# Optimization experiments

Hardware: AMD Instinct MI355X
Metric: run time of the kernel (lower is better)

## Reference

```python
import jax, jax.numpy as jnp
import numpy as np

VOCAB = 29
VEC = 512      # vector_dim
HID = 1024     # hidden_size
SEN = 64       # sen_len (== seq length)
BATCH = 2048


def setup_inputs() -> dict:
    key = jax.random.key(0)
    k1, k2, k3, k4, k5, k6 = jax.random.split(key, 6)
    s_emb = 1.0
    s_ih = 1.0 / np.sqrt(HID)
    s_cls = 1.0 / np.sqrt(HID)
    return {
        "x": jax.random.randint(k1, (BATCH, SEN), 0, VOCAB, dtype=jnp.int64),
        "emb": jax.random.normal(k2, (VOCAB, VEC), dtype=jnp.float32) * s_emb,
        "W_ih": jax.random.uniform(k3, (HID, VEC), dtype=jnp.float32, minval=-s_ih, maxval=s_ih),
        "W_hh": jax.random.uniform(k4, (HID, HID), dtype=jnp.float32, minval=-s_ih, maxval=s_ih),
        "W_cls": jax.random.uniform(k5, (SEN + 1, HID), dtype=jnp.float32, minval=-s_cls, maxval=s_cls),
        "b_cls": jax.random.uniform(k6, (SEN + 1,), dtype=jnp.float32, minval=-s_cls, maxval=s_cls),
    }


def reference(x, emb, W_ih, W_hh, W_cls, b_cls):
    # Embedding lookup: [B, S, VEC]
    xe = emb[x]
    # Precompute input projections for all timesteps: [B, S, HID]
    xin = jnp.einsum("bsv,hv->bsh", xe, W_ih)

    def step(h, x_t):
        # h: [B, HID], x_t: [B, HID] (already W_ih @ x)
        h_new = jnp.tanh(x_t + h @ W_hh.T)
        return h_new, None

    h0 = jnp.zeros((x.shape[0], HID), dtype=xin.dtype)
    h_last, _ = jax.lax.scan(step, h0, jnp.swapaxes(xin, 0, 1))  # scan over S

    # h.squeeze() in torch (num_layers=1) -> [B, HID]
    logits = h_last @ W_cls.T + b_cls  # [B, SEN+1]
    return logits
```

## Files before the change

### kernel.cpp

```cpp
#include <hip/hip_runtime.h>
#include <hip/hip_bf16.h>

#define VOCAB 29
#define VEC   512
#define HID   1024
#define SEN   64
#define BATCH 2048

typedef __bf16 bf16_t;
typedef bf16_t bf16x8 __attribute__((ext_vector_type(8)));
typedef float  floatx4 __attribute__((ext_vector_type(4)));

__global__ void cvt_whh(const float* __restrict__ w, bf16_t* __restrict__ o, int n) {
    int i = blockIdx.x * blockDim.x + threadIdx.x;
    if (i < n) o[i] = (bf16_t)w[i];
}

__global__ void cvt_wcls(const float* __restrict__ w, bf16_t* __restrict__ o) {
    int i = blockIdx.x * blockDim.x + threadIdx.x;
    if (i >= 80 * HID) return;
    o[i] = (i < 65 * HID) ? (bf16_t)w[i] : (bf16_t)0.0f;
}

__global__ void proj_kernel(const float* __restrict__ emb, const float* __restrict__ wih,
                            float* __restrict__ proj) {
    int idx = blockIdx.x * blockDim.x + threadIdx.x;
    if (idx >= VOCAB * HID) return;
    int v = idx / HID, h = idx % HID;
    const float* e = emb + v * VEC;
    const float* w = wih + h * VEC;
    float s = 0.f;
    for (int k = 0; k < VEC; k += 4) {
        float4 ev = *(const float4*)(e + k);
        float4 wv = *(const float4*)(w + k);
        s += ev.x * wv.x + ev.y * wv.y + ev.z * wv.z + ev.w * wv.w;
    }
    proj[idx] = s;
}

__device__ __forceinline__ float fast_tanh(float x) {
    float e = __expf(2.0f * x);
    return 1.0f - 2.0f / (e + 1.0f);
}

__device__ __forceinline__ void load16_to_lds(const bf16_t* g, bf16_t* l) {
    auto gp = reinterpret_cast<const __attribute__((address_space(1))) unsigned int*>(
        reinterpret_cast<uintptr_t>(g));
    auto lp = reinterpret_cast<__attribute__((address_space(3))) unsigned int*>(
        static_cast<unsigned int>(reinterpret_cast<uintptr_t>(l)));
    __builtin_amdgcn_global_load_lds(gp, lp, 16, 0, 0);
}

#define BM 128
#define BN 64
#define PANEL_BLKS 16
#define SB() __builtin_amdgcn_sched_barrier(0)

#define ISSUE_AF(BUF, KBASE)                                                     \
    _Pragma("unroll")                                                            \
    for (int j = 0; j < 8; j++) {                                                \
        af[BUF][j][0] = *(const bf16x8*)(hA + ((KBASE) + j) * 32);               \
        af[BUF][j][1] = *(const bf16x8*)(hA + 16 * HID + ((KBASE) + j) * 32);    \
    }

#define COMPUTE_GROUP(BUF, KBASE)                                                \
    _Pragma("unroll")                                                            \
    for (int j = 0; j < 8; j++) {                                                \
        const int p = (4 * ((KBASE) + j) + q) ^ l7;   \
        bf16x8 b0 = *(const bf16x8*)&Bsh[l16][p * 8];                            \
        bf16x8 b1 = *(const bf16x8*)&Bsh[16 + l16][p * 8];                       \
        bf16x8 b2 = *(const bf16x8*)&Bsh[32 + l16][p * 8];                       \
        bf16x8 b3 = *(const bf16x8*)&Bsh[48 + l16][p * 8];                       \
        acc[0][0] = __builtin_amdgcn_mfma_f32_16x16x32_bf16(af[BUF][j][0], b0, acc[0][0], 0, 0, 0); \
        acc[0][1] = __builtin_amdgcn_mfma_f32_16x16x32_bf16(af[BUF][j][0], b1, acc[0][1], 0, 0, 0); \
        acc[0][2] = __builtin_amdgcn_mfma_f32_16x16x32_bf16(af[BUF][j][0], b2, acc[0][2], 0, 0, 0); \
        acc[0][3] = __builtin_amdgcn_mfma_f32_16x16x32_bf16(af[BUF][j][0], b3, acc[0][3], 0, 0, 0); \
        acc[1][0] = __builtin_amdgcn_mfma_f32_16x16x32_bf16(af[BUF][j][1], b0, acc[1][0], 0, 0, 0); \
        acc[1][1] = __builtin_amdgcn_mfma_f32_16x16x32_bf16(af[BUF][j][1], b1, acc[1][1], 0, 0, 0); \
        acc[1][2] = __builtin_amdgcn_mfma_f32_16x16x32_bf16(af[BUF][j][1], b2, acc[1][2], 0, 0, 0); \
        acc[1][3] = __builtin_amdgcn_mfma_f32_16x16x32_bf16(af[BUF][j][1], b3, acc[1][3], 0, 0, 0); \
    }

__global__ __launch_bounds__(256, 1)
void rnn_persist(const bf16_t* __restrict__ whh, const float* __restrict__ proj,
                 const int* __restrict__ x, bf16_t* hbuf, int* scnt)
{
    __shared__ __align__(16) bf16_t Bsh[BN][HID];
    __shared__ int uni_sh;

    const int tid  = threadIdx.x;
    const int m0   = blockIdx.x * BM;
    const int n0   = blockIdx.y * BN;
    const int wave = tid >> 6;
    const int lane = tid & 63;
    const int wm   = wave * 32;
    const int q    = lane >> 4;
    const int l16  = lane & 15;
    const int l7   = l16 & 7;

    int* cnt   = scnt + blockIdx.x * 64;
    int* xmask = scnt + (16 + blockIdx.x) * 64;
    int* fl    = scnt + 2048 + blockIdx.x * 64;

#pragma unroll
    for (int half = 0; half < 2; half++)
#pragma unroll
        for (int it = 0; it < 16; it++) {
            const int r = it * 4 + wave;
            load16_to_lds(whh + (n0 + r) * HID + half * 512 + (lane ^ (r & 7)) * 8,
                          &Bsh[r][half * 512 + lane * 8]);
        }

    int rowl[8];
#pragma unroll
    for (int mi = 0; mi < 2; mi++)
#pragma unroll
        for (int r = 0; r < 4; r++) rowl[mi * 4 + r] = m0 + wm + mi * 16 + q * 4 + r;

    {
        float pv0[8][4];
#pragma unroll
        for (int i = 0; i < 8; i++) {
            const int tok = x[rowl[i] * SEN + 0];
            const float* pr = proj + tok * HID + n0;
#pragma unroll
            for (int ni = 0; ni < 4; ni++) pv0[i][ni] = pr[ni * 16 + l16];
        }
#pragma unroll
        for (int i = 0; i < 8; i++)
#pragma unroll
            for (int ni = 0; ni < 4; ni++)
                hbuf[rowl[i] * HID + n0 + ni * 16 + l16] = (bf16_t)fast_tanh(pv0[i][ni]);
    }

    int tk[8];
#pragma unroll
    for (int i = 0; i < 8; i++) tk[i] = x[rowl[i] * SEN + 1];

    __syncthreads();
    if (tid == 0) {
        const int my_xcd = (int)__builtin_amdgcn_s_getreg((3 << 11) | 20);
        __hip_atomic_fetch_or(xmask, 1 << my_xcd, __ATOMIC_RELAXED, __HIP_MEMORY_SCOPE_AGENT);
        __hip_atomic_fetch_add(cnt, 1, __ATOMIC_RELEASE, __HIP_MEMORY_SCOPE_AGENT);
        while (__hip_atomic_load(cnt, __ATOMIC_ACQUIRE, __HIP_MEMORY_SCOPE_AGENT) < PANEL_BLKS)
            __builtin_amdgcn_s_sleep(1);
        const int m = __hip_atomic_load(xmask, __ATOMIC_RELAXED, __HIP_MEMORY_SCOPE_AGENT);
        uni_sh = ((m & (m - 1)) == 0);
    }
    __syncthreads();
    asm volatile("buffer_inv" ::: "memory");
    const int safe = !uni_sh;

#pragma unroll 1
    for (int t = 1; t < SEN; t++) {
        const bf16_t* h_in  = hbuf + (size_t)((t + 1) & 1) * (BATCH * HID);
        bf16_t*       h_out = hbuf + (size_t)(t & 1) * (BATCH * HID);

        floatx4 acc[2][4];
#pragma unroll
        for (int i = 0; i < 2; i++)
#pragma unroll
            for (int j = 0; j < 4; j++) acc[i][j] = (floatx4){0.f, 0.f, 0.f, 0.f};

        const bf16_t* hA = h_in + (m0 + wm + l16) * HID + q * 8;
        bf16x8 af[2][8][2];

        ISSUE_AF(0, 0)
        ISSUE_AF(1, 8)
        float pv[8][4];
#pragma unroll
        for (int i = 0; i < 8; i++) {
            const float* pr = proj + tk[i] * HID + n0;
#pragma unroll
            for (int ni = 0; ni < 4; ni++) pv[i][ni] = pr[ni * 16 + l16];
        }
        SB();
        COMPUTE_GROUP(0, 0)
        SB();
        ISSUE_AF(0, 16)
        SB();
        COMPUTE_GROUP(1, 8)
        SB();
        ISSUE_AF(1, 24)
        if (t < SEN - 1) {
#pragma unroll
            for (int i = 0; i < 8; i++) tk[i] = x[rowl[i] * SEN + t + 1];
        }
        SB();
        COMPUTE_GROUP(0, 16)
        SB();
        COMPUTE_GROUP(1, 24)
        SB();

#pragma unroll
        for (int mi = 0; mi < 2; mi++)
#pragma unroll
            for (int r = 0; r < 4; r++)
#pragma unroll
                for (int ni = 0; ni < 4; ni++) {
                    float v = acc[mi][ni][r] + pv[mi * 4 + r][ni];
                    h_out[rowl[mi * 4 + r] * HID + n0 + ni * 16 + l16] = (bf16_t)fast_tanh(v);
                }

        if (t < SEN - 1) {
            __syncthreads();
            if (safe) {
                if (tid == 0) {
                    __hip_atomic_fetch_add(cnt, 1, __ATOMIC_RELEASE, __HIP_MEMORY_SCOPE_AGENT);
                    while (__hip_atomic_load(cnt, __ATOMIC_ACQUIRE, __HIP_MEMORY_SCOPE_AGENT)
                           < PANEL_BLKS * (t + 1))
                        __builtin_amdgcn_s_sleep(1);
                }
            } else {
                if (tid == 0)
                    __hip_atomic_store(&fl[blockIdx.y], t,
                                       __ATOMIC_RELAXED, __HIP_MEMORY_SCOPE_AGENT);
                if (tid < 16) {
                    while (__hip_atomic_load(&fl[tid],
                                             __ATOMIC_RELAXED, __HIP_MEMORY_SCOPE_AGENT) < t) {}
                }
            }
            __syncthreads();
            asm volatile("buffer_inv" ::: "memory");
        }
    }
}

#undef ISSUE_AF
#undef COMPUTE_GROUP

#define CBM 128
#define CLDK 72
__global__ __launch_bounds__(256)
void classifier_mfma(const bf16_t* __restrict__ h, const bf16_t* __restrict__ wcls,
                     const float* __restrict__ bcls, float* __restrict__ out)
{
    __shared__ __align__(16) bf16_t Ash[CBM][CLDK];
    __shared__ __align__(16) bf16_t Bsh[80][CLDK];

    const int tid = threadIdx.x;
    const int m0 = blockIdx.x * CBM;
    const int wave = tid >> 6, lane = tid & 63;
    const int wm = wave * 32;
    const int q = lane >> 4, l16 = lane & 15;

    floatx4 acc[2][5];
#pragma unroll
    for (int i = 0; i < 2; i++)
#pragma unroll
        for (int j = 0; j < 5; j++) acc[i][j] = (floatx4){0.f, 0.f, 0.f, 0.f};

    for (int kk = 0; kk < HID; kk += 64) {
#pragma unroll
        for (int it = 0; it < 4; it++) {
            int idx = tid + it * 256, r = idx >> 3, c = (idx & 7) * 8;
            *(uint4*)&Ash[r][c] = *(const uint4*)&h[(m0 + r) * HID + kk + c];
        }
#pragma unroll
        for (int it = 0; it < 3; it++) {
            int idx = tid + it * 256;
            if (idx < 640) {
                int r = idx >> 3, c = (idx & 7) * 8;
                *(uint4*)&Bsh[r][c] = *(const uint4*)&wcls[r * HID + kk + c];
            }
        }
        __syncthreads();
#pragma unroll
        for (int ks = 0; ks < 64; ks += 32) {
            bf16x8 af[2], bfr[5];
#pragma unroll
            for (int mi = 0; mi < 2; mi++)
                af[mi] = *(const bf16x8*)&Ash[wm + mi * 16 + l16][ks + q * 8];
#pragma unroll
            for (int ni = 0; ni < 5; ni++)
                bfr[ni] = *(const bf16x8*)&Bsh[ni * 16 + l16][ks + q * 8];
#pragma unroll
            for (int mi = 0; mi < 2; mi++)
#pragma unroll
                for (int ni = 0; ni < 5; ni++)
                    acc[mi][ni] = __builtin_amdgcn_mfma_f32_16x16x32_bf16(
                        af[mi], bfr[ni], acc[mi][ni], 0, 0, 0);
        }
        __syncthreads();
    }

#pragma unroll
    for (int mi = 0; mi < 2; mi++) {
#pragma unroll
        for (int r = 0; r < 4; r++) {
            int gm = m0 + wm + mi * 16 + q * 4 + r;
#pragma unroll
            for (int ni = 0; ni < 5; ni++) {
                int gn = ni * 16 + l16;
                if (gn < SEN + 1)
                    out[gm * (SEN + 1) + gn] = acc[mi][ni][r] + bcls[gn];
            }
        }
    }
}

extern "C" void kernel_launch(void* const* d_in, const int* in_sizes, int n_in,
                              void* d_out, int out_size, void* d_ws, size_t ws_size,
                              hipStream_t stream)
{
    const int*   x     = (const int*)  d_in[0];
    const float* emb   = (const float*)d_in[1];
    const float* w_ih  = (const float*)d_in[2];
    const float* w_hh  = (const float*)d_in[3];
    const float* w_cls = (const float*)d_in[4];
    const float* b_cls = (const float*)d_in[5];
    float* out = (float*)d_out;

    char* ws = (char*)d_ws;
    bf16_t* whh_bf  = (bf16_t*)ws;
    float*  proj    = (float*)(ws + (2u << 20));
    bf16_t* wcls_bf = (bf16_t*)(ws + (2u << 20) + (128u << 10));
    bf16_t* h0      = (bf16_t*)(ws + (2u << 20) + (288u << 10));
    bf16_t* h1      = (bf16_t*)(ws + (6u << 20) + (288u << 10));
    int*    scnt    = (int*)   (ws + (10u << 20) + (288u << 10));

    hipMemsetAsync(scnt, 0, 16384, stream);
    cvt_whh<<<(HID * HID) / 256, 256, 0, stream>>>(w_hh, whh_bf, HID * HID);
    proj_kernel<<<(VOCAB * HID + 255) / 256, 256, 0, stream>>>(emb, w_ih, proj);
    cvt_wcls<<<(80 * HID) / 256, 256, 0, stream>>>(w_cls, wcls_bf);

    dim3 grid(BATCH / BM, HID / BN);
    rnn_persist<<<grid, 256, 0, stream>>>(whh_bf, proj, x, h0, scnt);

    classifier_mfma<<<BATCH / CBM, 256, 0, stream>>>(h1, wcls_bf, b_cls, out);
}
```

Measured before the change: 756.9 us.

## Replace per-step panel barrier with per-group dataflow flags in persistent RNN

```diff
diff --git a/kernel.cpp b/kernel.cpp
--- a/kernel.cpp
+++ b/kernel.cpp
@@ -51,34 +51,40 @@
     __builtin_amdgcn_global_load_lds(gp, lp, 16, 0, 0);
 }
 
+__device__ __forceinline__ int flag_ld(const int* p) {
+    return __hip_atomic_load(p, __ATOMIC_RELAXED, __HIP_MEMORY_SCOPE_AGENT);
+}
+
 #define BM 128
 #define BN 64
 #define PANEL_BLKS 16
 #define SB() __builtin_amdgcn_sched_barrier(0)
 
-#define ISSUE_AF(BUF, KBASE)                                                     \
-    _Pragma("unroll")                                                            \
-    for (int j = 0; j < 8; j++) {                                                \
-        af[BUF][j][0] = *(const bf16x8*)(hA + ((KBASE) + j) * 32);               \
-        af[BUF][j][1] = *(const bf16x8*)(hA + 16 * HID + ((KBASE) + j) * 32);    \
-    }
-
-#define COMPUTE_GROUP(BUF, KBASE)                                                \
-    _Pragma("unroll")                                                            \
-    for (int j = 0; j < 8; j++) {                                                \
-        const int p = (4 * ((KBASE) + j) + q) ^ l7;   \
-        bf16x8 b0 = *(const bf16x8*)&Bsh[l16][p * 8];                            \
-        bf16x8 b1 = *(const bf16x8*)&Bsh[16 + l16][p * 8];                       \
-        bf16x8 b2 = *(const bf16x8*)&Bsh[32 + l16][p * 8];                       \
-        bf16x8 b3 = *(const bf16x8*)&Bsh[48 + l16][p * 8];                       \
-        acc[0][0] = __builtin_amdgcn_mfma_f32_16x16x32_bf16(af[BUF][j][0], b0, acc[0][0], 0, 0, 0); \
-        acc[0][1] = __builtin_amdgcn_mfma_f32_16x16x32_bf16(af[BUF][j][0], b1, acc[0][1], 0, 0, 0); \
-        acc[0][2] = __builtin_amdgcn_mfma_f32_16x16x32_bf16(af[BUF][j][0], b2, acc[0][2], 0, 0, 0); \
-        acc[0][3] = __builtin_amdgcn_mfma_f32_16x16x32_bf16(af[BUF][j][0], b3, acc[0][3], 0, 0, 0); \
-        acc[1][0] = __builtin_amdgcn_mfma_f32_16x16x32_bf16(af[BUF][j][1], b0, acc[1][0], 0, 0, 0); \
-        acc[1][1] = __builtin_amdgcn_mfma_f32_16x16x32_bf16(af[BUF][j][1], b1, acc[1][1], 0, 0, 0); \
-        acc[1][2] = __builtin_amdgcn_mfma_f32_16x16x32_bf16(af[BUF][j][1], b2, acc[1][2], 0, 0, 0); \
-        acc[1][3] = __builtin_amdgcn_mfma_f32_16x16x32_bf16(af[BUF][j][1], b3, acc[1][3], 0, 0, 0); \
+#define LOAD_G(B, G) {                                               \
+    const int c0_ = 2 * (G);                                         \
+    afb[B][0] = *(const bf16x8*)(hA + c0_ * 32);                     \
+    afb[B][1] = *(const bf16x8*)(hA + 16 * HID + c0_ * 32);          \
+    afb[B][2] = *(const bf16x8*)(hA + (c0_ + 1) * 32);               \
+    afb[B][3] = *(const bf16x8*)(hA + 16 * HID + (c0_ + 1) * 32); }
+
+#define COMP_G(B, G)                                                 \
+    _Pragma("unroll")                                                \
+    for (int j = 0; j < 2; j++) {                                    \
+        const int c_ = 2 * (G) + j;                                  \
+        const int p_ = ((4 * c_ + q) ^ l7) * 8;                      \
+        bf16x8 b0 = *(const bf16x8*)&Bsh[l16][p_];                   \
+        bf16x8 b1 = *(const bf16x8*)&Bsh[16 + l16][p_];              \
+        bf16x8 b2 = *(const bf16x8*)&Bsh[32 + l16][p_];              \
+        bf16x8 b3 = *(const bf16x8*)&Bsh[48 + l16][p_];              \
+        bf16x8 a0 = afb[B][2 * j], a1 = afb[B][2 * j + 1];           \
+        acc[0][0] = __builtin_amdgcn_mfma_f32_16x16x32_bf16(a0, b0, acc[0][0], 0, 0, 0); \
+        acc[0][1] = __builtin_amdgcn_mfma_f32_16x16x32_bf16(a0, b1, acc[0][1], 0, 0, 0); \
+        acc[0][2] = __builtin_amdgcn_mfma_f32_16x16x32_bf16(a0, b2, acc[0][2], 0, 0, 0); \
+        acc[0][3] = __builtin_amdgcn_mfma_f32_16x16x32_bf16(a0, b3, acc[0][3], 0, 0, 0); \
+        acc[1][0] = __builtin_amdgcn_mfma_f32_16x16x32_bf16(a1, b0, acc[1][0], 0, 0, 0); \
+        acc[1][1] = __builtin_amdgcn_mfma_f32_16x16x32_bf16(a1, b1, acc[1][1], 0, 0, 0); \
+        acc[1][2] = __builtin_amdgcn_mfma_f32_16x16x32_bf16(a1, b2, acc[1][2], 0, 0, 0); \
+        acc[1][3] = __builtin_amdgcn_mfma_f32_16x16x32_bf16(a1, b3, acc[1][3], 0, 0, 0); \
     }
 
 __global__ __launch_bounds__(256, 1)
@@ -89,8 +95,9 @@
     __shared__ int uni_sh;
 
     const int tid  = threadIdx.x;
-    const int m0   = blockIdx.x * BM;
-    const int n0   = blockIdx.y * BN;
+    const int bx   = blockIdx.x, by = blockIdx.y;
+    const int m0   = bx * BM;
+    const int n0   = by * BN;
     const int wave = tid >> 6;
     const int lane = tid & 63;
     const int wm   = wave * 32;
@@ -98,9 +105,9 @@
     const int l16  = lane & 15;
     const int l7   = l16 & 7;
 
-    int* cnt   = scnt + blockIdx.x * 64;
-    int* xmask = scnt + (16 + blockIdx.x) * 64;
-    int* fl    = scnt + 2048 + blockIdx.x * 64;
+    int* cnt   = scnt + bx * 64;
+    int* xmask = scnt + (16 + bx) * 64;
+    int* fl    = scnt + (32 + bx) * 64;
 
 #pragma unroll
     for (int half = 0; half < 2; half++)
@@ -139,6 +146,7 @@
 
     __syncthreads();
     if (tid == 0) {
+        __hip_atomic_store(&fl[by], 1, __ATOMIC_RELAXED, __HIP_MEMORY_SCOPE_AGENT);
         const int my_xcd = (int)__builtin_amdgcn_s_getreg((3 << 11) | 20);
         __hip_atomic_fetch_or(xmask, 1 << my_xcd, __ATOMIC_RELAXED, __HIP_MEMORY_SCOPE_AGENT);
         __hip_atomic_fetch_add(cnt, 1, __ATOMIC_RELEASE, __HIP_MEMORY_SCOPE_AGENT);
@@ -149,7 +157,7 @@
     }
     __syncthreads();
     asm volatile("buffer_inv" ::: "memory");
-    const int safe = !uni_sh;
+    const int fast = uni_sh;
 
 #pragma unroll 1
     for (int t = 1; t < SEN; t++) {
@@ -163,10 +171,14 @@
             for (int j = 0; j < 4; j++) acc[i][j] = (floatx4){0.f, 0.f, 0.f, 0.f};
 
         const bf16_t* hA = h_in + (m0 + wm + l16) * HID + q * 8;
-        bf16x8 af[2][8][2];
-
-        ISSUE_AF(0, 0)
-        ISSUE_AF(1, 8)
+        bf16x8 afb[2][4];
+
+        LOAD_G(0, by)
+        {
+            const int g1 = (by + 1) & 15;
+            if (fast) { while (flag_ld(&fl[g1]) < t) {} }
+            LOAD_G(1, g1)
+        }
         float pv[8][4];
 #pragma unroll
         for (int i = 0; i < 8; i++) {
@@ -174,23 +186,25 @@
 #pragma unroll
             for (int ni = 0; ni < 4; ni++) pv[i][ni] = pr[ni * 16 + l16];
         }
-        SB();
-        COMPUTE_GROUP(0, 0)
-        SB();
-        ISSUE_AF(0, 16)
-        SB();
-        COMPUTE_GROUP(1, 8)
-        SB();
-        ISSUE_AF(1, 24)
-        if (t < SEN - 1) {
-#pragma unroll
-            for (int i = 0; i < 8; i++) tk[i] = x[rowl[i] * SEN + t + 1];
-        }
-        SB();
-        COMPUTE_GROUP(0, 16)
-        SB();
-        COMPUTE_GROUP(1, 24)
-        SB();
+
+#pragma unroll
+        for (int i = 0; i < 16; i++) {
+            const int g   = (by + i) & 15;
+            const int gn2 = (by + i + 2) & 15;
+            int fv = t;
+            if (i < 14 && fast) fv = flag_ld(&fl[gn2]);
+            SB();
+            COMP_G(i & 1, g)
+            SB();
+            if (i < 14) {
+                if (fast) { while (fv < t) fv = flag_ld(&fl[gn2]); }
+                LOAD_G(i & 1, gn2)
+            }
+            if (i == 13 && t < SEN - 1) {
+#pragma unroll
+                for (int ii = 0; ii < 8; ii++) tk[ii] = x[rowl[ii] * SEN + t + 1];
+            }
+        }
 
 #pragma unroll
         for (int mi = 0; mi < 2; mi++)
@@ -204,30 +218,26 @@
 
         if (t < SEN - 1) {
             __syncthreads();
-            if (safe) {
+            if (fast) {
+                if (tid == 0)
+                    __hip_atomic_store(&fl[by], t + 1,
+                                       __ATOMIC_RELAXED, __HIP_MEMORY_SCOPE_AGENT);
+            } else {
                 if (tid == 0) {
                     __hip_atomic_fetch_add(cnt, 1, __ATOMIC_RELEASE, __HIP_MEMORY_SCOPE_AGENT);
                     while (__hip_atomic_load(cnt, __ATOMIC_ACQUIRE, __HIP_MEMORY_SCOPE_AGENT)
                            < PANEL_BLKS * (t + 1))
                         __builtin_amdgcn_s_sleep(1);
                 }
-            } else {
-                if (tid == 0)
-                    __hip_atomic_store(&fl[blockIdx.y], t,
-                                       __ATOMIC_RELAXED, __HIP_MEMORY_SCOPE_AGENT);
-                if (tid < 16) {
-                    while (__hip_atomic_load(&fl[tid],
-                                             __ATOMIC_RELAXED, __HIP_MEMORY_SCOPE_AGENT) < t) {}
-                }
-            }
-            __syncthreads();
+                __syncthreads();
+            }
             asm volatile("buffer_inv" ::: "memory");
         }
     }
 }
 
-#undef ISSUE_AF
-#undef COMPUTE_GROUP
+#undef LOAD_G
+#undef COMP_G
 
 #define CBM 128
 #define CLDK 72
```

Result: slower. 858.4 us (+13.4%).
